# Optimization experiments

Hardware: AMD Instinct MI355X
Metric: run time of the kernel (lower is better)

Reference implementation:

```python
import jax, jax.numpy as jnp
import numpy as np

N_NODES = 50000


def _segment_mean(vals, seg_ids, num_segments):
    s = jax.ops.segment_sum(vals, seg_ids, num_segments=num_segments)
    cnt = jax.ops.segment_sum(jnp.ones((vals.shape[0],), vals.dtype), seg_ids,
                              num_segments=num_segments)
    return s / jnp.clip(cnt, 1.0)[:, None]


def _sage_layer(h, src, dst, W_self, W_neigh, b):
    # mean-aggregate neighbor messages: gather h[src], scatter-mean to dst
    neigh = _segment_mean(h[src], dst, N_NODES)
    return h @ W_self + neigh @ W_neigh + b


def _edge_score(h, src, dst, Wp, bp):
    # concat(h_u, h_v) @ Wp == h_u @ Wp[:d] + h_v @ Wp[d:]
    d = h.shape[1]
    return h[src] @ Wp[:d] + h[dst] @ Wp[d:] + bp


def setup_inputs() -> dict:
    key = jax.random.key(0)
    ks = jax.random.split(key, 16)
    N, E, EP, EN = N_NODES, 800000, 200000, 200000
    d_in, d_hid, d_out = 128, 256, 128
    inp = {
        'x': jax.random.normal(ks[0], (N, d_in), jnp.float32),
        'msg_src': jax.random.randint(ks[1], (E,), 0, N, jnp.int32),
        'msg_dst': jax.random.randint(ks[2], (E,), 0, N, jnp.int32),
        'pos_src': jax.random.randint(ks[3], (EP,), 0, N, jnp.int32),
        'pos_dst': jax.random.randint(ks[4], (EP,), 0, N, jnp.int32),
        'neg_src': jax.random.randint(ks[5], (EN,), 0, N, jnp.int32),
        'neg_dst': jax.random.randint(ks[6], (EN,), 0, N, jnp.int32),
        'W1_self': jax.random.normal(ks[7], (d_in, d_hid), jnp.float32) * 0.05,
        'W1_neigh': jax.random.normal(ks[8], (d_in, d_hid), jnp.float32) * 0.05,
        'b1': jnp.zeros((d_hid,), jnp.float32),
        'W2_self': jax.random.normal(ks[9], (d_hid, d_out), jnp.float32) * 0.05,
        'W2_neigh': jax.random.normal(ks[10], (d_hid, d_out), jnp.float32) * 0.05,
        'b2': jnp.zeros((d_out,), jnp.float32),
        'Wp': jax.random.normal(ks[11], (2 * d_out, 1), jnp.float32) * 0.05,
        'bp': jnp.zeros((1,), jnp.float32),
    }
    return inp


def reference(x, msg_src, msg_dst, pos_src, pos_dst, neg_src, neg_dst,
              W1_self, W1_neigh, b1, W2_self, W2_neigh, b2, Wp, bp):
    h = _sage_layer(x, msg_src, msg_dst, W1_self, W1_neigh, b1)
    h = jax.nn.relu(h)
    h = _sage_layer(h, msg_src, msg_dst, W2_self, W2_neigh, b2)
    pos_score = _edge_score(h, pos_src, pos_dst, Wp, bp)
    neg_score = _edge_score(h, neg_src, neg_dst, Wp, bp)
    return pos_score, neg_score
```

## Files before the change

kernel.cpp:

```cpp
#include <hip/hip_runtime.h>


#define NN 50000
#define EM 800000
#define EPOS 200000
#define ENEG 200000
#define NB 196
#define CAP 8192
#define RPB 4096
#define CBLK 196
#define MTILES 3125
#define GEMM_GRID 1024
#define XCONV 6250
#define BT 1024

typedef __bf16 bf16;
typedef bf16 bf16x4 __attribute__((ext_vector_type(4)));
typedef bf16 bf16x8 __attribute__((ext_vector_type(8)));
typedef float floatx4 __attribute__((ext_vector_type(4)));

#define I_CNT  0
#define I_OFF  38416
#define I_ROW  76832
#define I_REND 127008
#define I_CSR  177184
#define B_CREG 7131264
#define B_XB   10331264
#define B_AGG1 23131264
#define B_H1   35931264
#define B_NV   61531264
#define B_WT1  62331264
#define B_WT2  62462336
#define B_P    62593408
#define B_Q    62793408

__global__ __launch_bounds__(256) void convbin_kernel(
    const float* __restrict__ x, bf16* __restrict__ xb,
    const float* __restrict__ W1s, const float* __restrict__ W1n,
    const float* __restrict__ W2n, const float* __restrict__ W2s,
    bf16* __restrict__ Wt1, bf16* __restrict__ Wt2,
    const int* __restrict__ msrc, const int* __restrict__ mdst,
    unsigned* __restrict__ creg, int* __restrict__ cntM,
    int* __restrict__ offM) {
    if (blockIdx.x < XCONV) {
        int i = blockIdx.x * 256 + threadIdx.x;
        float4 v = ((const float4*)x)[i];
        bf16x4 o;
        o[0] = (bf16)v.x; o[1] = (bf16)v.y; o[2] = (bf16)v.z; o[3] = (bf16)v.w;
        *(bf16x4*)(xb + (size_t)i * 4) = o;
    } else if (blockIdx.x < XCONV + 256) {
        int i = (blockIdx.x - XCONV) * 256 + threadIdx.x;
        int n = i >> 8, k = i & 255;
        float w1 = (k < 128) ? W1s[k * 256 + n] : W1n[(k - 128) * 256 + n];
        Wt1[i] = (bf16)w1;
        float w2 = (n < 128) ? W2n[k * 128 + n] : W2s[k * 128 + (n - 128)];
        Wt2[i] = (bf16)w2;
    } else {
        __shared__ int hist[NB];
        __shared__ int cnt2[NB];
        __shared__ int base[256];
        __shared__ unsigned sorted[RPB];
        int t = threadIdx.x;
        int cb = blockIdx.x - (XCONV + 256);
        int e0 = cb * RPB;
        int nrec = EM - e0; if (nrec > RPB) nrec = RPB;

        for (int i = t; i < NB; i += 256) { hist[i] = 0; cnt2[i] = 0; }
        __syncthreads();

        int myb[16];
        unsigned myrec[16];
#pragma unroll
        for (int j = 0; j < 16; ++j) {
            int idx = j * 256 + t;
            if (idx < nrec) {
                int s = msrc[e0 + idx], d = mdst[e0 + idx];
                myb[j] = d >> 8;
                myrec[j] = ((unsigned)(d & 255) << 16) | (unsigned)s;
                atomicAdd(&hist[myb[j]], 1);
            } else myb[j] = -1;
        }
        __syncthreads();

        base[t] = (t < NB) ? hist[t] : 0;
        __syncthreads();
        for (int o = 1; o < 256; o <<= 1) {
            int u = (t >= o) ? base[t - o] : 0;
            __syncthreads();
            base[t] += u;
            __syncthreads();
        }

#pragma unroll
        for (int j = 0; j < 16; ++j) {
            if (myb[j] >= 0) {
                int rk = atomicAdd(&cnt2[myb[j]], 1);
                int slot = base[myb[j]] - hist[myb[j]] + rk;
                sorted[slot] = myrec[j];
            }
        }
        __syncthreads();

        if (t < NB) {
            cntM[t * CBLK + cb] = hist[t];
            offM[t * CBLK + cb] = base[t] - hist[t];
        }
#pragma unroll
        for (int j = 0; j < 16; ++j) {
            int idx = j * 256 + t;
            if (idx < nrec) creg[(size_t)cb * RPB + idx] = sorted[idx];
        }
    }
}

__global__ __launch_bounds__(1024) void bsort_kernel(
    const unsigned* __restrict__ creg, const int* __restrict__ cntM,
    const int* __restrict__ offM, int* __restrict__ rowstart,
    int* __restrict__ rowend, int* __restrict__ csr) {
    __shared__ unsigned lrec[CAP];
    __shared__ unsigned lsrc[CAP];
    __shared__ int ccnt[256];
    __shared__ int cpos[256];
    __shared__ int coff[256];
    __shared__ int lhist[256];
    __shared__ int sc[256];
    __shared__ int lcur[256];
    int b = blockIdx.x, t = threadIdx.x;

    if (t < 256) {
        int cc = 0, oo = 0;
        if (t < CBLK) { cc = cntM[b * CBLK + t]; oo = offM[b * CBLK + t]; }
        ccnt[t] = cc; cpos[t] = cc; coff[t] = oo; lhist[t] = 0;
    }
    __syncthreads();
    for (int o = 1; o < 256; o <<= 1) {
        int u = (t < 256 && t >= o) ? cpos[t - o] : 0;
        __syncthreads();
        if (t < 256) cpos[t] += u;
        __syncthreads();
    }

    int wid = t >> 6, lane = t & 63;
    for (int cb = wid; cb < CBLK; cb += 16) {
        int c = ccnt[cb], ofs = coff[cb], d0 = cpos[cb] - c;
        for (int i = lane; i < c; i += 64) {
            unsigned rec = creg[(size_t)cb * RPB + ofs + i];
            lrec[d0 + i] = rec;
            atomicAdd(&lhist[(int)(rec >> 16) & 255], 1);
        }
    }
    __syncthreads();
    int cntb = cpos[255];

    if (t < 256) sc[t] = lhist[t];
    __syncthreads();
    for (int o = 1; o < 256; o <<= 1) {
        int u = (t < 256 && t >= o) ? sc[t - o] : 0;
        __syncthreads();
        if (t < 256) sc[t] += u;
        __syncthreads();
    }
    if (t < 256) {
        int node = b * 256 + t;
        if (node < NN) {
            rowstart[node] = b * CAP + sc[t] - lhist[t];
            rowend[node] = b * CAP + sc[t];
        }
        lcur[t] = sc[t] - lhist[t];
    }
    __syncthreads();

    for (int i = t; i < cntb; i += BT) {
        unsigned rec = lrec[i];
        int slot = atomicAdd(&lcur[(int)(rec >> 16) & 255], 1);
        lsrc[slot] = rec & 0xffffu;
    }
    __syncthreads();
    for (int i = t; i < cntb; i += BT) csr[b * CAP + i] = (int)lsrc[i];
}

__global__ __launch_bounds__(256) void gather1_kernel(const bf16* __restrict__ feat,
                                                      const int* __restrict__ rowstart,
                                                      const int* __restrict__ rowend,
                                                      const int* __restrict__ csr,
                                                      bf16* __restrict__ agg) {
    int node = (blockIdx.x * 256 + threadIdx.x) >> 6;
    if (node >= NN) return;
    int lane = threadIdx.x & 63;
    int q = lane >> 4, r = lane & 15;
    int c = r * 8;
    int beg = rowstart[node], end = rowend[node];
    float a0[8] = {0.f, 0.f, 0.f, 0.f, 0.f, 0.f, 0.f, 0.f};
    float a1[8] = {0.f, 0.f, 0.f, 0.f, 0.f, 0.f, 0.f, 0.f};
    float a2[8] = {0.f, 0.f, 0.f, 0.f, 0.f, 0.f, 0.f, 0.f};
    float a3[8] = {0.f, 0.f, 0.f, 0.f, 0.f, 0.f, 0.f, 0.f};
    int i = beg + q;
    for (; i + 12 < end; i += 16) {
        int s0 = csr[i], s1 = csr[i + 4], s2 = csr[i + 8], s3 = csr[i + 12];
        bf16x8 v0 = *(const bf16x8*)(feat + (size_t)s0 * 128 + c);
        bf16x8 v1 = *(const bf16x8*)(feat + (size_t)s1 * 128 + c);
        bf16x8 v2 = *(const bf16x8*)(feat + (size_t)s2 * 128 + c);
        bf16x8 v3 = *(const bf16x8*)(feat + (size_t)s3 * 128 + c);
#pragma unroll
        for (int u = 0; u < 8; ++u) {
            a0[u] += (float)v0[u];
            a1[u] += (float)v1[u];
            a2[u] += (float)v2[u];
            a3[u] += (float)v3[u];
        }
    }
    for (; i < end; i += 4) {
        int s0 = csr[i];
        bf16x8 v0 = *(const bf16x8*)(feat + (size_t)s0 * 128 + c);
#pragma unroll
        for (int u = 0; u < 8; ++u) a0[u] += (float)v0[u];
    }
#pragma unroll
    for (int u = 0; u < 8; ++u) a0[u] += a1[u] + a2[u] + a3[u];
#pragma unroll
    for (int m = 16; m <= 32; m <<= 1)
#pragma unroll
        for (int u = 0; u < 8; ++u) a0[u] += __shfl_xor(a0[u], m);
    if (q == 0) {
        int deg = end - beg;
        float inv = 1.0f / (float)(deg > 0 ? deg : 1);
        bf16x8 o;
#pragma unroll
        for (int u = 0; u < 8; ++u) o[u] = (bf16)(a0[u] * inv);
        *(bf16x8*)(agg + (size_t)node * 128 + c) = o;
    }
}

__global__ __launch_bounds__(256) void gemm1_kernel(
    const bf16* __restrict__ xb, const bf16* __restrict__ aggb,
    const bf16* __restrict__ Wt, const float* __restrict__ b1,
    bf16* __restrict__ h1b) {
    int w = threadIdx.x >> 6;
    int lane = threadIdx.x & 63;
    int r = lane & 15, quad = lane >> 4;
    int colbase = w * 64;

    bf16x8 bfr[4][8];
#pragma unroll
    for (int t = 0; t < 4; ++t)
#pragma unroll
        for (int kk = 0; kk < 8; ++kk)
            bfr[t][kk] = *(const bf16x8*)(Wt + (size_t)(colbase + t * 16 + r) * 256
                                          + kk * 32 + quad * 8);
    float bb[4];
#pragma unroll
    for (int t = 0; t < 4; ++t) bb[t] = b1[colbase + t * 16 + r];

    for (int tile = blockIdx.x; tile < MTILES; tile += GEMM_GRID) {
        int m0 = tile * 16;
        int row = m0 + r;
        bf16x8 a[8];
#pragma unroll
        for (int kk = 0; kk < 4; ++kk)
            a[kk] = *(const bf16x8*)(xb + (size_t)row * 128 + kk * 32 + quad * 8);
#pragma unroll
        for (int kk = 4; kk < 8; ++kk)
            a[kk] = *(const bf16x8*)(aggb + (size_t)row * 128 + (kk - 4) * 32 + quad * 8);
        floatx4 acc[4];
#pragma unroll
        for (int t = 0; t < 4; ++t) acc[t] = (floatx4){0.f, 0.f, 0.f, 0.f};
#pragma unroll
        for (int kk = 0; kk < 8; ++kk)
#pragma unroll
            for (int t = 0; t < 4; ++t)
                acc[t] = __builtin_amdgcn_mfma_f32_16x16x32_bf16(a[kk], bfr[t][kk],
                                                                 acc[t], 0, 0, 0);
        int mb = m0 + quad * 4;
#pragma unroll
        for (int t = 0; t < 4; ++t) {
            int col = colbase + t * 16 + r;
#pragma unroll
            for (int rr = 0; rr < 4; ++rr) {
                float v = acc[t][rr] + bb[t];
                v = v > 0.f ? v : 0.f;
                h1b[(size_t)(mb + rr) * 256 + col] = (bf16)v;
            }
        }
    }
}

__global__ __launch_bounds__(256) void gemm2_kernel(
    const bf16* __restrict__ h1b, const bf16* __restrict__ Wt,
    const float* __restrict__ b2, const float* __restrict__ wp,
    float4* __restrict__ nodev) {
    __shared__ float lp[4][16];
    __shared__ float lq[4][16];
    int w = threadIdx.x >> 6;
    int lane = threadIdx.x & 63;
    int r = lane & 15, quad = lane >> 4;
    int colbase = w * 64;

    bf16x8 bfr[4][8];
#pragma unroll
    for (int t = 0; t < 4; ++t)
#pragma unroll
        for (int kk = 0; kk < 8; ++kk)
            bfr[t][kk] = *(const bf16x8*)(Wt + (size_t)(colbase + t * 16 + r) * 256
                                          + kk * 32 + quad * 8);
    float bb[4], wA[4], wB[4];
#pragma unroll
    for (int t = 0; t < 4; ++t) {
        int col = colbase + t * 16 + r;
        if (w < 2) {
            bb[t] = 0.f;
            wA[t] = wp[col];
            wB[t] = wp[128 + col];
        } else {
            int c2 = col - 128;
            bb[t] = b2[c2];
            wA[t] = wp[c2];
            wB[t] = wp[128 + c2];
        }
    }

    for (int tile = blockIdx.x; tile < MTILES; tile += GEMM_GRID) {
        int m0 = tile * 16;
        int row = m0 + r;
        bf16x8 a[8];
#pragma unroll
        for (int kk = 0; kk < 8; ++kk)
            a[kk] = *(const bf16x8*)(h1b + (size_t)row * 256 + kk * 32 + quad * 8);
        floatx4 acc[4];
#pragma unroll
        for (int t = 0; t < 4; ++t) acc[t] = (floatx4){0.f, 0.f, 0.f, 0.f};
#pragma unroll
        for (int kk = 0; kk < 8; ++kk)
#pragma unroll
            for (int t = 0; t < 4; ++t)
                acc[t] = __builtin_amdgcn_mfma_f32_16x16x32_bf16(a[kk], bfr[t][kk],
                                                                 acc[t], 0, 0, 0);
        float pacc[4], qacc[4];
#pragma unroll
        for (int rr = 0; rr < 4; ++rr) {
            float pr = 0.f, qr = 0.f;
#pragma unroll
            for (int t = 0; t < 4; ++t) {
                float v = acc[t][rr] + bb[t];
                pr += v * wA[t];
                qr += v * wB[t];
            }
            pacc[rr] = pr;
            qacc[rr] = qr;
        }
#pragma unroll
        for (int m = 1; m <= 8; m <<= 1) {
#pragma unroll
            for (int rr = 0; rr < 4; ++rr) {
                pacc[rr] += __shfl_xor(pacc[rr], m);
                qacc[rr] += __shfl_xor(qacc[rr], m);
            }
        }
        if (r == 0) {
#pragma unroll
            for (int rr = 0; rr < 4; ++rr) {
                lp[w][quad * 4 + rr] = pacc[rr];
                lq[w][quad * 4 + rr] = qacc[rr];
            }
        }
        __syncthreads();
        if (threadIdx.x < 16) {
            int rw = threadIdx.x;
            float4 o;
            o.x = lp[0][rw] + lp[1][rw];
            o.y = lq[0][rw] + lq[1][rw];
            o.z = lp[2][rw] + lp[3][rw];
            o.w = lq[2][rw] + lq[3][rw];
            nodev[m0 + rw] = o;
        }
        __syncthreads();
    }
}

__global__ __launch_bounds__(256) void gather2_kernel(
    const float4* __restrict__ nodev, const int* __restrict__ rowstart,
    const int* __restrict__ rowend, const int* __restrict__ csr,
    float* __restrict__ p, float* __restrict__ q) {
    int t = threadIdx.x;
    int node = blockIdx.x * 16 + (t >> 4);
    if (node >= NN) return;
    int l = t & 15;
    int beg = rowstart[node], end = rowend[node];
    float pz = 0.f, qz = 0.f;
    for (int i = beg + l; i < end; i += 16) {
        float4 v = nodev[csr[i]];
        pz += v.x;
        qz += v.y;
    }
#pragma unroll
    for (int m = 8; m >= 1; m >>= 1) {
        pz += __shfl_xor(pz, m);
        qz += __shfl_xor(qz, m);
    }
    if (l == 0) {
        int deg = end - beg;
        float inv = 1.0f / (float)(deg > 0 ? deg : 1);
        float4 me = nodev[node];
        p[node] = me.z + pz * inv;
        q[node] = me.w + qz * inv;
    }
}

__global__ __launch_bounds__(256) void score_kernel(
    const int* __restrict__ psrc, const int* __restrict__ pdst,
    const int* __restrict__ nsrc, const int* __restrict__ ndst,
    const float* __restrict__ p, const float* __restrict__ q,
    const float* __restrict__ bp, float* __restrict__ out) {
    int i = blockIdx.x * blockDim.x + threadIdx.x;
    float b = bp[0];
    if (i < EPOS) {
        out[i] = p[psrc[i]] + q[pdst[i]] + b;
    } else if (i < EPOS + ENEG) {
        int j = i - EPOS;
        out[i] = p[nsrc[j]] + q[ndst[j]] + b;
    }
}

extern "C" void kernel_launch(void* const* d_in, const int* in_sizes, int n_in,
                              void* d_out, int out_size, void* d_ws, size_t ws_size,
                              hipStream_t stream) {
    const float* x    = (const float*)d_in[0];
    const int*   msrc = (const int*)d_in[1];
    const int*   mdst = (const int*)d_in[2];
    const int*   psrc = (const int*)d_in[3];
    const int*   pdst = (const int*)d_in[4];
    const int*   nsrc = (const int*)d_in[5];
    const int*   ndst = (const int*)d_in[6];
    const float* W1s  = (const float*)d_in[7];
    const float* W1n  = (const float*)d_in[8];
    const float* b1   = (const float*)d_in[9];
    const float* W2s  = (const float*)d_in[10];
    const float* W2n  = (const float*)d_in[11];
    const float* b2   = (const float*)d_in[12];
    const float* wp   = (const float*)d_in[13];
    const float* bp   = (const float*)d_in[14];

    char* ws = (char*)d_ws;
    int*   cntM     = (int*)ws + I_CNT;
    int*   offM     = (int*)ws + I_OFF;
    int*   rowstart = (int*)ws + I_ROW;
    int*   rowend   = (int*)ws + I_REND;
    int*   csr      = (int*)ws + I_CSR;
    unsigned* creg  = (unsigned*)(ws + B_CREG);
    bf16*  xb    = (bf16*)(ws + B_XB);
    bf16*  agg1b = (bf16*)(ws + B_AGG1);
    bf16*  h1b   = (bf16*)(ws + B_H1);
    float4* nodev = (float4*)(ws + B_NV);
    bf16*  Wt1   = (bf16*)(ws + B_WT1);
    bf16*  Wt2   = (bf16*)(ws + B_WT2);
    float* p     = (float*)(ws + B_P);
    float* q     = (float*)(ws + B_Q);
    float* out   = (float*)d_out;

    convbin_kernel<<<XCONV + 256 + CBLK, 256, 0, stream>>>(
        x, xb, W1s, W1n, W2n, W2s, Wt1, Wt2, msrc, mdst, creg, cntM, offM);
    bsort_kernel<<<NB, BT, 0, stream>>>(creg, cntM, offM, rowstart, rowend, csr);
    gather1_kernel<<<(NN + 3) / 4, 256, 0, stream>>>(xb, rowstart, rowend, csr, agg1b);
    gemm1_kernel<<<GEMM_GRID, 256, 0, stream>>>(xb, agg1b, Wt1, b1, h1b);
    gemm2_kernel<<<GEMM_GRID, 256, 0, stream>>>(h1b, Wt2, b2, wp, nodev);
    gather2_kernel<<<(NN + 15) / 16, 256, 0, stream>>>(nodev, rowstart, rowend, csr, p, q);
    score_kernel<<<(EPOS + ENEG + 255) / 256, 256, 0, stream>>>(
        psrc, pdst, nsrc, ndst, p, q, bp, out);
}
```

Before: 233.2 us.

## Fuse bucket sort with layer-1 gather using quarter-bucket blocks

Replaces the per-bucket sort kernel (196 blocks of 1024 threads) with 784 blocks of 512 threads, each handling a quarter of a 256-node bucket. Each block filters records by quarter using ballot-based compaction, builds the CSR segment in shared memory, and then does the layer-1 neighbor mean aggregation directly from the shared-memory source list, removing a separate gather kernel launch and the CSR re-read. Every block now scans all records of its bucket, so record reads go up fourfold, and the capacity of each quarter is limited to 2048 entries. The GEMM grid is also halved.

Measured after the change: 241.4 us. 1.04x slower.

```diff
diff --git a/kernel.cpp b/kernel.cpp
--- a/kernel.cpp
+++ b/kernel.cpp
@@ -7,12 +7,12 @@
 #define ENEG 200000
 #define NB 196
 #define CAP 8192
+#define QCAP 2048
 #define RPB 4096
 #define CBLK 196
 #define MTILES 3125
-#define GEMM_GRID 1024
+#define GEMM_GRID 512
 #define XCONV 6250
-#define BT 1024
 
 typedef __bf16 bf16;
 typedef bf16 bf16x4 __attribute__((ext_vector_type(4)));
@@ -113,121 +113,129 @@
     }
 }
 
-__global__ __launch_bounds__(1024) void bsort_kernel(
+__global__ __launch_bounds__(512) void qbucket_kernel(
     const unsigned* __restrict__ creg, const int* __restrict__ cntM,
     const int* __restrict__ offM, int* __restrict__ rowstart,
-    int* __restrict__ rowend, int* __restrict__ csr) {
-    __shared__ unsigned lrec[CAP];
-    __shared__ unsigned lsrc[CAP];
-    __shared__ int ccnt[256];
-    __shared__ int cpos[256];
-    __shared__ int coff[256];
-    __shared__ int lhist[256];
-    __shared__ int sc[256];
-    __shared__ int lcur[256];
-    int b = blockIdx.x, t = threadIdx.x;
-
-    if (t < 256) {
-        int cc = 0, oo = 0;
-        if (t < CBLK) { cc = cntM[b * CBLK + t]; oo = offM[b * CBLK + t]; }
-        ccnt[t] = cc; cpos[t] = cc; coff[t] = oo; lhist[t] = 0;
-    }
+    int* __restrict__ rowend, int* __restrict__ csr,
+    const bf16* __restrict__ feat, bf16* __restrict__ agg) {
+    __shared__ unsigned lrec[QCAP];
+    __shared__ unsigned lsrc[QCAP];
+    __shared__ int ccnt[CBLK];
+    __shared__ int coff[CBLK];
+    __shared__ int lhist[64];
+    __shared__ int ssc[64];
+    __shared__ int lcur[64];
+    __shared__ int lcnt;
+    int t = threadIdx.x;
+    int cb = blockIdx.x >> 2, qt = blockIdx.x & 3;
+
+    if (t < CBLK) { ccnt[t] = cntM[cb * CBLK + t]; coff[t] = offM[cb * CBLK + t]; }
+    if (t < 64) lhist[t] = 0;
+    if (t == 0) lcnt = 0;
     __syncthreads();
-    for (int o = 1; o < 256; o <<= 1) {
-        int u = (t < 256 && t >= o) ? cpos[t - o] : 0;
-        __syncthreads();
-        if (t < 256) cpos[t] += u;
-        __syncthreads();
-    }
 
     int wid = t >> 6, lane = t & 63;
-    for (int cb = wid; cb < CBLK; cb += 16) {
-        int c = ccnt[cb], ofs = coff[cb], d0 = cpos[cb] - c;
-        for (int i = lane; i < c; i += 64) {
-            unsigned rec = creg[(size_t)cb * RPB + ofs + i];
-            lrec[d0 + i] = rec;
-            atomicAdd(&lhist[(int)(rec >> 16) & 255], 1);
+    for (int ch = wid; ch < CBLK; ch += 8) {
+        int cc = ccnt[ch], ofs = coff[ch];
+        for (int i0 = 0; i0 < cc; i0 += 64) {
+            int i = i0 + lane;
+            unsigned rec = 0;
+            bool keep = false;
+            if (i < cc) {
+                rec = creg[(size_t)ch * RPB + ofs + i];
+                keep = (int)((rec >> 22) & 3u) == qt;
+            }
+            unsigned long long m = __ballot(keep);
+            int base = 0;
+            if (lane == 0) {
+                int cnt = __popcll(m);
+                base = cnt ? atomicAdd(&lcnt, cnt) : 0;
+            }
+            base = __shfl(base, 0);
+            if (keep) {
+                int pos = base + __popcll(m & ((1ULL << lane) - 1ULL));
+                lrec[pos] = rec;
+                atomicAdd(&lhist[(rec >> 16) & 63], 1);
+            }
         }
     }
     __syncthreads();
-    int cntb = cpos[255];
-
-    if (t < 256) sc[t] = lhist[t];
+    int total = lcnt;
+
+    if (t < 64) ssc[t] = lhist[t];
     __syncthreads();
-    for (int o = 1; o < 256; o <<= 1) {
-        int u = (t < 256 && t >= o) ? sc[t - o] : 0;
-        __syncthreads();
-        if (t < 256) sc[t] += u;
-        __syncthreads();
-    }
-    if (t < 256) {
-        int node = b * 256 + t;
+    for (int o = 1; o < 64; o <<= 1) {
+        int u = (t < 64 && t >= o) ? ssc[t - o] : 0;
+        __syncthreads();
+        if (t < 64) ssc[t] += u;
+        __syncthreads();
+    }
+    int cbase = cb * CAP + qt * QCAP;
+    if (t < 64) {
+        lcur[t] = ssc[t] - lhist[t];
+        int node = cb * 256 + qt * 64 + t;
         if (node < NN) {
-            rowstart[node] = b * CAP + sc[t] - lhist[t];
-            rowend[node] = b * CAP + sc[t];
-        }
-        lcur[t] = sc[t] - lhist[t];
+            rowstart[node] = cbase + ssc[t] - lhist[t];
+            rowend[node]   = cbase + ssc[t];
+        }
     }
     __syncthreads();
 
-    for (int i = t; i < cntb; i += BT) {
+    for (int i = t; i < total; i += 512) {
         unsigned rec = lrec[i];
-        int slot = atomicAdd(&lcur[(int)(rec >> 16) & 255], 1);
+        int slot = atomicAdd(&lcur[(rec >> 16) & 63], 1);
         lsrc[slot] = rec & 0xffffu;
     }
     __syncthreads();
-    for (int i = t; i < cntb; i += BT) csr[b * CAP + i] = (int)lsrc[i];
-}
-
-__global__ __launch_bounds__(256) void gather1_kernel(const bf16* __restrict__ feat,
-                                                      const int* __restrict__ rowstart,
-                                                      const int* __restrict__ rowend,
-                                                      const int* __restrict__ csr,
-                                                      bf16* __restrict__ agg) {
-    int node = (blockIdx.x * 256 + threadIdx.x) >> 6;
-    if (node >= NN) return;
-    int lane = threadIdx.x & 63;
+    for (int i = t; i < total; i += 512) csr[cbase + i] = (int)lsrc[i];
+
     int q = lane >> 4, r = lane & 15;
     int c = r * 8;
-    int beg = rowstart[node], end = rowend[node];
-    float a0[8] = {0.f, 0.f, 0.f, 0.f, 0.f, 0.f, 0.f, 0.f};
-    float a1[8] = {0.f, 0.f, 0.f, 0.f, 0.f, 0.f, 0.f, 0.f};
-    float a2[8] = {0.f, 0.f, 0.f, 0.f, 0.f, 0.f, 0.f, 0.f};
-    float a3[8] = {0.f, 0.f, 0.f, 0.f, 0.f, 0.f, 0.f, 0.f};
-    int i = beg + q;
-    for (; i + 12 < end; i += 16) {
-        int s0 = csr[i], s1 = csr[i + 4], s2 = csr[i + 8], s3 = csr[i + 12];
-        bf16x8 v0 = *(const bf16x8*)(feat + (size_t)s0 * 128 + c);
-        bf16x8 v1 = *(const bf16x8*)(feat + (size_t)s1 * 128 + c);
-        bf16x8 v2 = *(const bf16x8*)(feat + (size_t)s2 * 128 + c);
-        bf16x8 v3 = *(const bf16x8*)(feat + (size_t)s3 * 128 + c);
-#pragma unroll
-        for (int u = 0; u < 8; ++u) {
-            a0[u] += (float)v0[u];
-            a1[u] += (float)v1[u];
-            a2[u] += (float)v2[u];
-            a3[u] += (float)v3[u];
-        }
-    }
-    for (; i < end; i += 4) {
-        int s0 = csr[i];
-        bf16x8 v0 = *(const bf16x8*)(feat + (size_t)s0 * 128 + c);
-#pragma unroll
-        for (int u = 0; u < 8; ++u) a0[u] += (float)v0[u];
-    }
-#pragma unroll
-    for (int u = 0; u < 8; ++u) a0[u] += a1[u] + a2[u] + a3[u];
-#pragma unroll
-    for (int m = 16; m <= 32; m <<= 1)
-#pragma unroll
-        for (int u = 0; u < 8; ++u) a0[u] += __shfl_xor(a0[u], m);
-    if (q == 0) {
-        int deg = end - beg;
-        float inv = 1.0f / (float)(deg > 0 ? deg : 1);
-        bf16x8 o;
-#pragma unroll
-        for (int u = 0; u < 8; ++u) o[u] = (bf16)(a0[u] * inv);
-        *(bf16x8*)(agg + (size_t)node * 128 + c) = o;
+    for (int k = 0; k < 8; ++k) {
+        int ln = wid * 8 + k;
+        int node = cb * 256 + qt * 64 + ln;
+        if (node >= NN) break;
+        int beg = ssc[ln] - lhist[ln], end = ssc[ln];
+        float a0[8] = {0.f, 0.f, 0.f, 0.f, 0.f, 0.f, 0.f, 0.f};
+        float a1[8] = {0.f, 0.f, 0.f, 0.f, 0.f, 0.f, 0.f, 0.f};
+        float a2[8] = {0.f, 0.f, 0.f, 0.f, 0.f, 0.f, 0.f, 0.f};
+        float a3[8] = {0.f, 0.f, 0.f, 0.f, 0.f, 0.f, 0.f, 0.f};
+        int i = beg + q;
+        for (; i + 12 < end; i += 16) {
+            int s0 = (int)lsrc[i], s1 = (int)lsrc[i + 4];
+            int s2 = (int)lsrc[i + 8], s3 = (int)lsrc[i + 12];
+            bf16x8 v0 = *(const bf16x8*)(feat + (size_t)s0 * 128 + c);
+            bf16x8 v1 = *(const bf16x8*)(feat + (size_t)s1 * 128 + c);
+            bf16x8 v2 = *(const bf16x8*)(feat + (size_t)s2 * 128 + c);
+            bf16x8 v3 = *(const bf16x8*)(feat + (size_t)s3 * 128 + c);
+#pragma unroll
+            for (int u = 0; u < 8; ++u) {
+                a0[u] += (float)v0[u];
+                a1[u] += (float)v1[u];
+                a2[u] += (float)v2[u];
+                a3[u] += (float)v3[u];
+            }
+        }
+        for (; i < end; i += 4) {
+            int s0 = (int)lsrc[i];
+            bf16x8 v0 = *(const bf16x8*)(feat + (size_t)s0 * 128 + c);
+#pragma unroll
+            for (int u = 0; u < 8; ++u) a0[u] += (float)v0[u];
+        }
+#pragma unroll
+        for (int u = 0; u < 8; ++u) a0[u] += a1[u] + a2[u] + a3[u];
+#pragma unroll
+        for (int m = 16; m <= 32; m <<= 1)
+#pragma unroll
+            for (int u = 0; u < 8; ++u) a0[u] += __shfl_xor(a0[u], m);
+        if (q == 0) {
+            int deg = end - beg;
+            float inv = 1.0f / (float)(deg > 0 ? deg : 1);
+            bf16x8 o;
+#pragma unroll
+            for (int u = 0; u < 8; ++u) o[u] = (bf16)(a0[u] * inv);
+            *(bf16x8*)(agg + (size_t)node * 128 + c) = o;
+        }
     }
 }
 
@@ -458,8 +466,8 @@
 
     convbin_kernel<<<XCONV + 256 + CBLK, 256, 0, stream>>>(
         x, xb, W1s, W1n, W2n, W2s, Wt1, Wt2, msrc, mdst, creg, cntM, offM);
-    bsort_kernel<<<NB, BT, 0, stream>>>(creg, cntM, offM, rowstart, rowend, csr);
-    gather1_kernel<<<(NN + 3) / 4, 256, 0, stream>>>(xb, rowstart, rowend, csr, agg1b);
+    qbucket_kernel<<<NB * 4, 512, 0, stream>>>(creg, cntM, offM, rowstart,
+                                               rowend, csr, xb, agg1b);
     gemm1_kernel<<<GEMM_GRID, 256, 0, stream>>>(xb, agg1b, Wt1, b1, h1b);
     gemm2_kernel<<<GEMM_GRID, 256, 0, stream>>>(h1b, Wt2, b2, wp, nodev);
     gather2_kernel<<<(NN + 15) / 16, 256, 0, stream>>>(nodev, rowstart, rowend, csr, p, q);
```
